# Kernel optimization log

Measured on AMD Instinct MI355X. Metric: run time of the kernel, lower is better.

Reference implementation:

```python
import jax, jax.numpy as jnp
import numpy as np

D_MODEL = 1024
HEADS = 16
D_K = D_MODEL // HEADS
D_FF = 4096
B, S = 8, 1024
EPS = 1e-5
NEG = -1e9


def layer_norm(x, g, b):
    mu = jnp.mean(x, axis=-1, keepdims=True)
    var = jnp.var(x, axis=-1, keepdims=True)
    return (x - mu) * jax.lax.rsqrt(var + EPS) * g + b


def setup_inputs() -> dict:
    key = jax.random.key(0)
    ks = jax.random.split(key, 10)
    sc = lambda d: 1.0 / np.sqrt(d)
    return {
        "x": jax.random.normal(ks[0], (B, S, D_MODEL), jnp.float32),
        "mask": jnp.ones((B, 1, 1, S), jnp.int32),
        "wq": jax.random.normal(ks[1], (D_MODEL, D_MODEL), jnp.float32) * sc(D_MODEL),
        "bq": jnp.zeros((D_MODEL,), jnp.float32),
        "wk": jax.random.normal(ks[2], (D_MODEL, D_MODEL), jnp.float32) * sc(D_MODEL),
        "bk": jnp.zeros((D_MODEL,), jnp.float32),
        "wv": jax.random.normal(ks[3], (D_MODEL, D_MODEL), jnp.float32) * sc(D_MODEL),
        "bv": jnp.zeros((D_MODEL,), jnp.float32),
        "wo": jax.random.normal(ks[4], (D_MODEL, D_MODEL), jnp.float32) * sc(D_MODEL),
        "bo": jnp.zeros((D_MODEL,), jnp.float32),
        "w1": jax.random.normal(ks[5], (D_MODEL, D_FF), jnp.float32) * sc(D_MODEL),
        "b1": jnp.zeros((D_FF,), jnp.float32),
        "w2": jax.random.normal(ks[6], (D_FF, D_MODEL), jnp.float32) * sc(D_FF),
        "b2": jnp.zeros((D_MODEL,), jnp.float32),
        "ln1_g": jnp.ones((D_MODEL,), jnp.float32),
        "ln1_b": jnp.zeros((D_MODEL,), jnp.float32),
        "ln2_g": jnp.ones((D_MODEL,), jnp.float32),
        "ln2_b": jnp.zeros((D_MODEL,), jnp.float32),
    }


def reference(x, mask, wq, bq, wk, bk, wv, bv, wo, bo, w1, b1, w2, b2,
              ln1_g, ln1_b, ln2_g, ln2_b):
    b, s, d = x.shape

    # --- self-attention sublayer with residual + LN (pre-norm, dropout=0) ---
    h = layer_norm(x, ln1_g, ln1_b)
    q = (h @ wq + bq).reshape(b, s, HEADS, D_K).transpose(0, 2, 1, 3)  # [b,h,s,dk]
    k = (h @ wk + bk).reshape(b, s, HEADS, D_K).transpose(0, 2, 1, 3)
    v = (h @ wv + bv).reshape(b, s, HEADS, D_K).transpose(0, 2, 1, 3)

    scores = jnp.einsum("bhqd,bhkd->bhqk", q, k) / np.sqrt(D_K)  # [b,h,s,s]
    scores = jnp.where(mask == 0, NEG, scores)
    attn = jax.nn.softmax(scores, axis=-1)
    ctx = jnp.einsum("bhqk,bhkd->bhqd", attn, v)
    ctx = ctx.transpose(0, 2, 1, 3).reshape(b, s, d)
    x = x + (ctx @ wo + bo)

    # --- feed-forward sublayer with residual + LN ---
    h2 = layer_norm(x, ln2_g, ln2_b)
    ff = jax.nn.relu(h2 @ w1 + b1) @ w2 + b2
    return x + ff
```

## Files before the change

kernel.cpp:

```cpp
#include <hip/hip_runtime.h>
#include <hip/hip_bf16.h>

typedef __attribute__((ext_vector_type(8))) __bf16 bf16x8;
typedef __attribute__((ext_vector_type(4))) __bf16 bf16x4;
typedef __attribute__((ext_vector_type(4))) float  f32x4;

__device__ __forceinline__ void gload_lds16(const __bf16* g, __bf16* l) {
    __builtin_amdgcn_global_load_lds(
        (const __attribute__((address_space(1))) void*)g,
        (__attribute__((address_space(3))) void*)l, 16, 0, 0);
}

__global__ __launch_bounds__(256) void transpose_all(
    const float* __restrict__ wq, const float* __restrict__ wk,
    const float* __restrict__ wv, const float* __restrict__ wo,
    const float* __restrict__ w1, const float* __restrict__ w2,
    __bf16* __restrict__ wqkvT, __bf16* __restrict__ woT,
    __bf16* __restrict__ w1T, __bf16* __restrict__ w2T) {
    __shared__ float t[32][33];
    const int bid = blockIdx.x;
    const float* in; __bf16* out; int K, N, nb, kb;
    if (bid < 4096) {
        const int which = bid >> 10, tt = bid & 1023;
        K = 1024; N = 1024;
        in  = which == 0 ? wq : which == 1 ? wk : which == 2 ? wv : wo;
        out = which == 3 ? woT : wqkvT + (size_t)which * 1048576;
        nb = (tt & 31) * 32; kb = (tt >> 5) * 32;
    } else if (bid < 8192) {
        const int tt = bid - 4096;
        in = w1; out = w1T; K = 1024; N = 4096;
        nb = (tt & 127) * 32; kb = (tt >> 7) * 32;
    } else {
        const int tt = bid - 8192;
        in = w2; out = w2T; K = 4096; N = 1024;
        nb = (tt & 31) * 32; kb = (tt >> 5) * 32;
    }
    const int tx = threadIdx.x & 31, ty = threadIdx.x >> 5;
#pragma unroll
    for (int i = 0; i < 32; i += 8)
        t[ty + i][tx] = in[(size_t)(kb + ty + i) * N + nb + tx];
    __syncthreads();
#pragma unroll
    for (int i = 0; i < 32; i += 8)
        out[(size_t)(nb + ty + i) * K + kb + tx] = (__bf16)t[tx][ty + i];
}

__global__ void concat3(const float* __restrict__ a, const float* __restrict__ b,
                        const float* __restrict__ c, float* __restrict__ o, int n) {
    int i = blockIdx.x * 256 + threadIdx.x;
    if (i < n) { o[i] = a[i]; o[n + i] = b[i]; o[2 * n + i] = c[i]; }
}

__global__ __launch_bounds__(256) void ln_to_bf16(const float* __restrict__ x,
                                                  const float* __restrict__ g,
                                                  const float* __restrict__ bb,
                                                  __bf16* __restrict__ out) {
    const int row = blockIdx.x, t = threadIdx.x;
    const float4 v = ((const float4*)(x + (size_t)row * 1024))[t];
    float s  = v.x + v.y + v.z + v.w;
    float ss = v.x * v.x + v.y * v.y + v.z * v.z + v.w * v.w;
#pragma unroll
    for (int off = 32; off; off >>= 1) {
        s  += __shfl_down(s, off);
        ss += __shfl_down(ss, off);
    }
    __shared__ float ps[4], pss[4];
    if ((t & 63) == 0) { ps[t >> 6] = s; pss[t >> 6] = ss; }
    __syncthreads();
    s  = ps[0] + ps[1] + ps[2] + ps[3];
    ss = pss[0] + pss[1] + pss[2] + pss[3];
    const float mu   = s * (1.0f / 1024.0f);
    const float var  = ss * (1.0f / 1024.0f) - mu * mu;
    const float rinv = rsqrtf(var + 1e-5f);
    const float4 gv = ((const float4*)g)[t];
    const float4 bv = ((const float4*)bb)[t];
    bf16x4 o;
    o[0] = (__bf16)((v.x - mu) * rinv * gv.x + bv.x);
    o[1] = (__bf16)((v.y - mu) * rinv * gv.y + bv.y);
    o[2] = (__bf16)((v.z - mu) * rinv * gv.z + bv.z);
    o[3] = (__bf16)((v.w - mu) * rinv * gv.w + bv.w);
    *(bf16x4*)(out + (size_t)row * 1024 + 4 * t) = o;
}

template <int MODE>
__global__ __launch_bounds__(512, 2) void gemm256(const __bf16* __restrict__ A,
                                                  const __bf16* __restrict__ BT,
                                                  const float* __restrict__ bias,
                                                  __bf16* __restrict__ outp,
                                                  int M, int N, int K, int NMB) {
    __shared__ __align__(16) __bf16 lds[65536];
    const int nwg = gridDim.x;
    const int bid = blockIdx.x;
    const int wgid = (bid & 7) * (nwg >> 3) + (bid >> 3);
    const int bm = (wgid % NMB) * 256, bn = (wgid / NMB) * 256;
    const int tid = threadIdx.x, l = tid & 63, w = tid >> 6;
    const int wm = (w >> 2) * 128, wn = (w & 3) * 64;
    const int lg = l >> 4, lm = l & 15;
    const int NT = K >> 6;

    const __bf16* gsrc[4];
    int ldst[4];
#pragma unroll
    for (int j = 0; j < 4; ++j) {
        const unsigned X = (unsigned)(((j & 1) << 13) + (w << 10) + l * 16);
        const unsigned L = X ^ (((X >> 7) & 7u) << 4);
        const int row = L >> 6, col = (L & 63) >> 1;
        gsrc[j] = (j < 2 ? A + (size_t)(bm + row) * K : BT + (size_t)(bn + row) * K) + col;
        ldst[j] = ((j < 2 ? 0 : 16384) + ((j & 1) << 13) + (w << 10)) >> 1;
    }
    int aoff[2][4], boff[4];
#pragma unroll
    for (int mh = 0; mh < 2; ++mh)
#pragma unroll
        for (int fr = 0; fr < 4; ++fr) {
            const unsigned Lb = (unsigned)(wm + mh * 64 + fr * 16 + lm) * 64 + lg * 16;
            aoff[mh][fr] = (int)(Lb ^ (((Lb >> 7) & 7u) << 4)) >> 1;
        }
#pragma unroll
    for (int n = 0; n < 4; ++n) {
        const unsigned Lb = (unsigned)(wn + n * 16 + lm) * 64 + lg * 16;
        boff[n] = (int)(16384u + (Lb ^ (((Lb >> 7) & 7u) << 4))) >> 1;
    }

    f32x4 acc[8][4];
#pragma unroll
    for (int m = 0; m < 8; ++m)
#pragma unroll
        for (int n = 0; n < 4; ++n) acc[m][n] = f32x4{0.f, 0.f, 0.f, 0.f};

#define ISSUE_SUB(u)                                                          \
    do {                                                                      \
        __bf16* sbp = lds + (((u) & 3) << 14);                                \
        const int go = (u) << 5;                                              \
        _Pragma("unroll")                                                     \
        for (int j = 0; j < 4; ++j) gload_lds16(gsrc[j] + go, sbp + ldst[j]); \
    } while (0)

#define MFMA16(MH, BREG)                                                      \
    do {                                                                      \
        __builtin_amdgcn_s_setprio(1);                                        \
        _Pragma("unroll")                                                     \
        for (int i = 0; i < 4; ++i)                                           \
            _Pragma("unroll")                                                 \
            for (int n = 0; n < 4; ++n)                                       \
                acc[(MH)*4 + i][n] = __builtin_amdgcn_mfma_f32_16x16x32_bf16( \
                    af[i], BREG[n], acc[(MH)*4 + i][n], 0, 0, 0);             \
        __builtin_amdgcn_s_setprio(0);                                        \
    } while (0)

    ISSUE_SUB(0); ISSUE_SUB(1); ISSUE_SUB(2); ISSUE_SUB(3);
    asm volatile("s_waitcnt vmcnt(8)" ::: "memory");
    __builtin_amdgcn_s_barrier();

    for (int t = 0; t < NT; ++t) {
        const int sa = ((2 * t) & 3) << 14, sb = ((2 * t + 1) & 3) << 14;
        bf16x8 af[4], b0[4], b1[4];
#pragma unroll
        for (int fr = 0; fr < 4; ++fr) af[fr] = *(const bf16x8*)(lds + sa + aoff[0][fr]);
#pragma unroll
        for (int n = 0; n < 4; ++n) b0[n] = *(const bf16x8*)(lds + sa + boff[n]);
        asm volatile("" ::: "memory");
        __builtin_amdgcn_s_barrier();
        __builtin_amdgcn_sched_barrier(0);
        MFMA16(0, b0);
        __builtin_amdgcn_sched_barrier(0);
        __builtin_amdgcn_s_barrier();
#pragma unroll
        for (int fr = 0; fr < 4; ++fr) af[fr] = *(const bf16x8*)(lds + sa + aoff[1][fr]);
        asm volatile("" ::: "memory");
        __builtin_amdgcn_s_barrier();
        __builtin_amdgcn_sched_barrier(0);
        MFMA16(1, b0);
        __builtin_amdgcn_sched_barrier(0);
        __builtin_amdgcn_s_barrier();
        if (t < NT - 2) ISSUE_SUB(2 * t + 4);
#pragma unroll
        for (int fr = 0; fr < 4; ++fr) af[fr] = *(const bf16x8*)(lds + sb + aoff[0][fr]);
#pragma unroll
        for (int n = 0; n < 4; ++n) b1[n] = *(const bf16x8*)(lds + sb + boff[n]);
        asm volatile("" ::: "memory");
        __builtin_amdgcn_s_barrier();
        __builtin_amdgcn_sched_barrier(0);
        MFMA16(0, b1);
        __builtin_amdgcn_sched_barrier(0);
        __builtin_amdgcn_s_barrier();
#pragma unroll
        for (int fr = 0; fr < 4; ++fr) af[fr] = *(const bf16x8*)(lds + sb + aoff[1][fr]);
        asm volatile("" ::: "memory");
        __builtin_amdgcn_s_barrier();
        __builtin_amdgcn_sched_barrier(0);
        MFMA16(1, b1);
        __builtin_amdgcn_sched_barrier(0);
        __builtin_amdgcn_s_barrier();
        if (t < NT - 2) {
            ISSUE_SUB(2 * t + 5);
            asm volatile("s_waitcnt vmcnt(8)" ::: "memory");
        } else if (t == NT - 2) {
            asm volatile("s_waitcnt vmcnt(0)" ::: "memory");
        }
        __builtin_amdgcn_s_barrier();
    }
#undef ISSUE_SUB
#undef MFMA16

#pragma unroll
    for (int m = 0; m < 8; ++m) {
        const int row = bm + wm + (m >> 2) * 64 + (m & 3) * 16 + lg * 4;
#pragma unroll
        for (int n = 0; n < 4; ++n) {
            const int col = bn + wn + n * 16 + lm;
            const float bvv = bias[col];
#pragma unroll
            for (int r = 0; r < 4; ++r) {
                const float v = acc[m][n][r] + bvv;
                outp[(size_t)(row + r) * N + col] =
                    (MODE == 1) ? (__bf16)fmaxf(v, 0.f) : (__bf16)v;
            }
        }
    }
}

__global__ __launch_bounds__(512, 2) void gemm256x128(const __bf16* __restrict__ A,
                                                      const __bf16* __restrict__ BT,
                                                      const float* __restrict__ bias,
                                                      const float* __restrict__ resid,
                                                      float* __restrict__ outp,
                                                      int M, int N, int K, int NMB) {
    __shared__ __align__(16) __bf16 lds[49152];
    const int nwg = gridDim.x;
    const int bid = blockIdx.x;
    const int wgid = (bid & 7) * (nwg >> 3) + (bid >> 3);
    const int bm = (wgid % NMB) * 256, bn = (wgid / NMB) * 128;
    const int tid = threadIdx.x, l = tid & 63, w = tid >> 6;
    const int wm = (w >> 1) * 64, wn = (w & 1) * 64;
    const int lg = l >> 4, lm = l & 15;
    const int NT = K >> 6;

    const __bf16* gsrc[3];
    int ldst[3];
#pragma unroll
    for (int j = 0; j < 3; ++j) {
        const unsigned X = (unsigned)((j == 1 ? 8192 : 0) + tid * 16);
        const unsigned L = X ^ (((X >> 7) & 7u) << 4);
        const int row = L >> 6, col = (L & 63) >> 1;
        gsrc[j] = (j < 2 ? A + (size_t)(bm + row) * K : BT + (size_t)(bn + row) * K) + col;
        ldst[j] = ((j < 2 ? (j << 13) : 16384) + (w << 10)) >> 1;
    }
    int aoff[2][2], boff[4];
#pragma unroll
    for (int mh = 0; mh < 2; ++mh)
#pragma unroll
        for (int fr = 0; fr < 2; ++fr) {
            const unsigned Lb = (unsigned)(wm + mh * 32 + fr * 16 + lm) * 64 + lg * 16;
            aoff[mh][fr] = (int)(Lb ^ (((Lb >> 7) & 7u) << 4)) >> 1;
        }
#pragma unroll
    for (int n = 0; n < 4; ++n) {
        const unsigned Lb = (unsigned)(wn + n * 16 + lm) * 64 + lg * 16;
        boff[n] = (int)(16384u + (Lb ^ (((Lb >> 7) & 7u) << 4))) >> 1;
    }

    f32x4 acc[4][4];
#pragma unroll
    for (int m = 0; m < 4; ++m)
#pragma unroll
        for (int n = 0; n < 4; ++n) acc[m][n] = f32x4{0.f, 0.f, 0.f, 0.f};

#define ISSUE_SUB(u)                                                          \
    do {                                                                      \
        __bf16* sbp = lds + ((u) & 3) * 12288;                                \
        const int go = (u) << 5;                                              \
        _Pragma("unroll")                                                     \
        for (int j = 0; j < 3; ++j) gload_lds16(gsrc[j] + go, sbp + ldst[j]); \
    } while (0)

#define MFMA8(MH, BREG)                                                       \
    do {                                                                      \
        __builtin_amdgcn_s_setprio(1);                                        \
        _Pragma("unroll")                                                     \
        for (int i = 0; i < 2; ++i)                                           \
            _Pragma("unroll")                                                 \
            for (int n = 0; n < 4; ++n)                                       \
                acc[(MH)*2 + i][n] = __builtin_amdgcn_mfma_f32_16x16x32_bf16( \
                    af[i], BREG[n], acc[(MH)*2 + i][n], 0, 0, 0);             \
        __builtin_amdgcn_s_setprio(0);                                        \
    } while (0)

    ISSUE_SUB(0); ISSUE_SUB(1); ISSUE_SUB(2); ISSUE_SUB(3);
    asm volatile("s_waitcnt vmcnt(6)" ::: "memory");
    __builtin_amdgcn_s_barrier();

    for (int t = 0; t < NT; ++t) {
        const int sa = ((2 * t) & 3) * 12288, sb = ((2 * t + 1) & 3) * 12288;
        bf16x8 af[2], b0[4], b1[4];
#pragma unroll
        for (int fr = 0; fr < 2; ++fr) af[fr] = *(const bf16x8*)(lds + sa + aoff[0][fr]);
#pragma unroll
        for (int n = 0; n < 4; ++n) b0[n] = *(const bf16x8*)(lds + sa + boff[n]);
        asm volatile("" ::: "memory");
        __builtin_amdgcn_s_barrier();
        __builtin_amdgcn_sched_barrier(0);
        MFMA8(0, b0);
        __builtin_amdgcn_sched_barrier(0);
        __builtin_amdgcn_s_barrier();
#pragma unroll
        for (int fr = 0; fr < 2; ++fr) af[fr] = *(const bf16x8*)(lds + sa + aoff[1][fr]);
        asm volatile("" ::: "memory");
        __builtin_amdgcn_s_barrier();
        __builtin_amdgcn_sched_barrier(0);
        MFMA8(1, b0);
        __builtin_amdgcn_sched_barrier(0);
        __builtin_amdgcn_s_barrier();
        if (t < NT - 2) ISSUE_SUB(2 * t + 4);
#pragma unroll
        for (int fr = 0; fr < 2; ++fr) af[fr] = *(const bf16x8*)(lds + sb + aoff[0][fr]);
#pragma unroll
        for (int n = 0; n < 4; ++n) b1[n] = *(const bf16x8*)(lds + sb + boff[n]);
        asm volatile("" ::: "memory");
        __builtin_amdgcn_s_barrier();
        __builtin_amdgcn_sched_barrier(0);
        MFMA8(0, b1);
        __builtin_amdgcn_sched_barrier(0);
        __builtin_amdgcn_s_barrier();
#pragma unroll
        for (int fr = 0; fr < 2; ++fr) af[fr] = *(const bf16x8*)(lds + sb + aoff[1][fr]);
        asm volatile("" ::: "memory");
        __builtin_amdgcn_s_barrier();
        __builtin_amdgcn_sched_barrier(0);
        MFMA8(1, b1);
        __builtin_amdgcn_sched_barrier(0);
        __builtin_amdgcn_s_barrier();
        if (t < NT - 2) {
            ISSUE_SUB(2 * t + 5);
            asm volatile("s_waitcnt vmcnt(6)" ::: "memory");
        } else if (t == NT - 2) {
            asm volatile("s_waitcnt vmcnt(0)" ::: "memory");
        }
        __builtin_amdgcn_s_barrier();
    }
#undef ISSUE_SUB
#undef MFMA8

#pragma unroll
    for (int m = 0; m < 4; ++m) {
        const int row = bm + wm + m * 16 + lg * 4;
#pragma unroll
        for (int n = 0; n < 4; ++n) {
            const int col = bn + wn + n * 16 + lm;
            const float bvv = bias[col];
#pragma unroll
            for (int r = 0; r < 4; ++r) {
                const size_t idx = (size_t)(row + r) * N + col;
                outp[idx] = resid[idx] + acc[m][n][r] + bvv;
            }
        }
    }
}

__global__ __launch_bounds__(512, 2) void gemm_qkv(const __bf16* __restrict__ A,
                                                   const __bf16* __restrict__ BT,
                                                   const float* __restrict__ bias,
                                                   __bf16* __restrict__ outp,
                                                   __bf16* __restrict__ vTout,
                                                   int M, int N, int K, int NMB) {
    __shared__ __align__(16) __bf16 lds[49152];
    const int nwg = gridDim.x;
    const int bid = blockIdx.x;
    const int wgid = (bid & 7) * (nwg >> 3) + (bid >> 3);
    const int bm = (wgid % NMB) * 128, bn = (wgid / NMB) * 256;
    const int tid = threadIdx.x, l = tid & 63, w = tid >> 6;
    const int wm = (w >> 2) * 64, wn = (w & 3) * 64;
    const int lg = l >> 4, lm = l & 15;
    const int NT = K >> 6;

    const __bf16* gsrc[3];
    int ldst[3];
#pragma unroll
    for (int j = 0; j < 3; ++j) {
        const unsigned X = (unsigned)((j == 0 ? 0 : (j - 1) * 8192) + tid * 16);
        const unsigned L = X ^ (((X >> 7) & 7u) << 4);
        const int row = L >> 6, col = (L & 63) >> 1;
        gsrc[j] = (j == 0 ? A + (size_t)(bm + row) * K : BT + (size_t)(bn + row) * K) + col;
        ldst[j] = ((j == 0 ? 0 : 8192 + (j - 1) * 8192) + (w << 10)) >> 1;
    }
    int aoff[2][2], boff[4];
#pragma unroll
    for (int mh = 0; mh < 2; ++mh)
#pragma unroll
        for (int fr = 0; fr < 2; ++fr) {
            const unsigned Lb = (unsigned)(wm + mh * 32 + fr * 16 + lm) * 64 + lg * 16;
            aoff[mh][fr] = (int)(Lb ^ (((Lb >> 7) & 7u) << 4)) >> 1;
        }
#pragma unroll
    for (int n = 0; n < 4; ++n) {
        const unsigned Lb = (unsigned)(wn + n * 16 + lm) * 64 + lg * 16;
        boff[n] = (int)(8192u + (Lb ^ (((Lb >> 7) & 7u) << 4))) >> 1;
    }

    f32x4 acc[4][4];
#pragma unroll
    for (int m = 0; m < 4; ++m)
#pragma unroll
        for (int n = 0; n < 4; ++n) acc[m][n] = f32x4{0.f, 0.f, 0.f, 0.f};

#define ISSUE_SUB(u)                                                          \
    do {                                                                      \
        __bf16* sbp = lds + ((u) & 3) * 12288;                                \
        const int go = (u) << 5;                                              \
        _Pragma("unroll")                                                     \
        for (int j = 0; j < 3; ++j) gload_lds16(gsrc[j] + go, sbp + ldst[j]); \
    } while (0)

#define MFMA8(MH, BREG)                                                       \
    do {                                                                      \
        __builtin_amdgcn_s_setprio(1);                                        \
        _Pragma("unroll")                                                     \
        for (int i = 0; i < 2; ++i)                                           \
            _Pragma("unroll")                                                 \
            for (int n = 0; n < 4; ++n)                                       \
                acc[(MH)*2 + i][n] = __builtin_amdgcn_mfma_f32_16x16x32_bf16( \
                    af[i], BREG[n], acc[(MH)*2 + i][n], 0, 0, 0);             \
        __builtin_amdgcn_s_setprio(0);                                        \
    } while (0)

    ISSUE_SUB(0); ISSUE_SUB(1); ISSUE_SUB(2); ISSUE_SUB(3);
    asm volatile("s_waitcnt vmcnt(6)" ::: "memory");
    __builtin_amdgcn_s_barrier();

    for (int t = 0; t < NT; ++t) {
        const int sa = ((2 * t) & 3) * 12288, sb = ((2 * t + 1) & 3) * 12288;
        bf16x8 af[2], b0[4], b1[4];
#pragma unroll
        for (int fr = 0; fr < 2; ++fr) af[fr] = *(const bf16x8*)(lds + sa + aoff[0][fr]);
#pragma unroll
        for (int n = 0; n < 4; ++n) b0[n] = *(const bf16x8*)(lds + sa + boff[n]);
        asm volatile("" ::: "memory");
        __builtin_amdgcn_s_barrier();
        __builtin_amdgcn_sched_barrier(0);
        MFMA8(0, b0);
        __builtin_amdgcn_sched_barrier(0);
        __builtin_amdgcn_s_barrier();
#pragma unroll
        for (int fr = 0; fr < 2; ++fr) af[fr] = *(const bf16x8*)(lds + sa + aoff[1][fr]);
        asm volatile("" ::: "memory");
        __builtin_amdgcn_s_barrier();
        __builtin_amdgcn_sched_barrier(0);
        MFMA8(1, b0);
        __builtin_amdgcn_sched_barrier(0);
        __builtin_amdgcn_s_barrier();
        if (t < NT - 2) ISSUE_SUB(2 * t + 4);
#pragma unroll
        for (int fr = 0; fr < 2; ++fr) af[fr] = *(const bf16x8*)(lds + sb + aoff[0][fr]);
#pragma unroll
        for (int n = 0; n < 4; ++n) b1[n] = *(const bf16x8*)(lds + sb + boff[n]);
        asm volatile("" ::: "memory");
        __builtin_amdgcn_s_barrier();
        __builtin_amdgcn_sched_barrier(0);
        MFMA8(0, b1);
        __builtin_amdgcn_sched_barrier(0);
        __builtin_amdgcn_s_barrier();
#pragma unroll
        for (int fr = 0; fr < 2; ++fr) af[fr] = *(const bf16x8*)(lds + sb + aoff[1][fr]);
        asm volatile("" ::: "memory");
        __builtin_amdgcn_s_barrier();
        __builtin_amdgcn_sched_barrier(0);
        MFMA8(1, b1);
        __builtin_amdgcn_sched_barrier(0);
        __builtin_amdgcn_s_barrier();
        if (t < NT - 2) {
            ISSUE_SUB(2 * t + 5);
            asm volatile("s_waitcnt vmcnt(6)" ::: "memory");
        } else if (t == NT - 2) {
            asm volatile("s_waitcnt vmcnt(0)" ::: "memory");
        }
        __builtin_amdgcn_s_barrier();
    }
#undef ISSUE_SUB
#undef MFMA8

    const bool isQ = bn < 1024;
#pragma unroll
    for (int m = 0; m < 4; ++m) {
        const int row = bm + wm + m * 16 + lg * 4;
#pragma unroll
        for (int n = 0; n < 4; ++n) {
            const int col = bn + wn + n * 16 + lm;
            const float bvv = bias[col];
            if (bn >= 2048) {
                bf16x4 o;
#pragma unroll
                for (int r = 0; r < 4; ++r) o[r] = (__bf16)(acc[m][n][r] + bvv);
                *(bf16x4*)(vTout + (size_t)((row >> 10) * 1024 + (col - 2048)) * 1024 +
                           (row & 1023)) = o;
            } else {
#pragma unroll
                for (int r = 0; r < 4; ++r) {
                    float v = acc[m][n][r] + bvv;
                    if (isQ) v *= 0.18033688f;
                    outp[(size_t)(row + r) * 2048 + col] = (__bf16)v;
                }
            }
        }
    }
}

__global__ __launch_bounds__(512) void attn_kernel(const __bf16* __restrict__ qk,
                                                   const __bf16* __restrict__ vT,
                                                   const int* __restrict__ mask,
                                                   __bf16* __restrict__ ctx) {
    const int qt = blockIdx.x, h = blockIdx.y, b = blockIdx.z;
    const int tid = threadIdx.x, w = tid >> 6, l = tid & 63;
    const int lg = l >> 4, lm = l & 15;

    __shared__ __align__(16) __bf16 Ks[2][64][76];
    __shared__ __align__(16) __bf16 Vt[2][64][76];
    __shared__ __align__(16) __bf16 Ps[8][16][76];

    const int qrow = qt * 128 + w * 16 + lm;
    const __bf16* qp = qk + (size_t)(b * 1024 + qrow) * 2048 + h * 64 + lg * 8;
    bf16x8 aq[2];
    aq[0] = *(const bf16x8*)qp;
    aq[1] = *(const bf16x8*)(qp + 32);

    const int r0 = tid >> 3, cc0 = (tid & 7) * 8;
    const __bf16* kbase = qk + (size_t)(b * 1024 + r0) * 2048 + 1024 + h * 64 + cc0;
    const __bf16* vbase = vT + (size_t)(b * 1024 + h * 64 + r0) * 1024 + cc0;
    uint4 kreg, vreg;
#define ALOAD(kt)                                                      \
    do {                                                               \
        kreg = *(const uint4*)(kbase + (size_t)(kt) * 64 * 2048);      \
        vreg = *(const uint4*)(vbase + (kt) * 64);                     \
    } while (0)
#define AWRITE(bf)                                                     \
    do {                                                               \
        *(uint4*)&Ks[bf][r0][cc0] = kreg;                              \
        *(uint4*)&Vt[bf][r0][cc0] = vreg;                              \
    } while (0)

    ALOAD(0); AWRITE(0); ALOAD(1);
    __syncthreads();

    const int* mbase = mask + b * 1024;
    float mrun = -1e30f, lsum = 0.f;
    f32x4 oacc[4];
#pragma unroll
    for (int n = 0; n < 4; ++n) oacc[n] = f32x4{0.f, 0.f, 0.f, 0.f};

    for (int kt = 0; kt < 16; ++kt) {
        const int cur = kt & 1;
        f32x4 sacc[4];
        int4 mk4[4];
#pragma unroll
        for (int n = 0; n < 4; ++n) {
            mk4[n] = *(const int4*)(mbase + kt * 64 + n * 16 + lg * 4);
            sacc[n] = f32x4{0.f, 0.f, 0.f, 0.f};
#pragma unroll
            for (int kk = 0; kk < 2; ++kk) {
                bf16x8 bk = *(const bf16x8*)&Ks[cur][n * 16 + lm][lg * 8 + kk * 32];
                sacc[n] = __builtin_amdgcn_mfma_f32_16x16x32_bf16(bk, aq[kk], sacc[n], 0, 0, 0);
            }
        }
        float p[4][4], mn[4];
#pragma unroll
        for (int n = 0; n < 4; ++n) {
            p[n][0] = mk4[n].x ? sacc[n][0] : -1e9f;
            p[n][1] = mk4[n].y ? sacc[n][1] : -1e9f;
            p[n][2] = mk4[n].z ? sacc[n][2] : -1e9f;
            p[n][3] = mk4[n].w ? sacc[n][3] : -1e9f;
            mn[n] = fmaxf(fmaxf(p[n][0], p[n][1]), fmaxf(p[n][2], p[n][3]));
        }
        float mloc = fmaxf(fmaxf(mn[0], mn[1]), fmaxf(mn[2], mn[3]));
        mloc = fmaxf(mloc, __shfl_xor(mloc, 16));
        mloc = fmaxf(mloc, __shfl_xor(mloc, 32));
        const float pm = fmaxf(mrun, mloc);
        if (!__all(pm - mrun <= 11.5f)) {
            const float sc = exp2f(mrun - pm);
            mrun = pm;
            lsum *= sc;
            float scr[4];
#pragma unroll
            for (int r = 0; r < 4; ++r) scr[r] = __shfl(sc, lg * 4 + r);
#pragma unroll
            for (int n = 0; n < 4; ++n)
#pragma unroll
                for (int r = 0; r < 4; ++r) oacc[n][r] *= scr[r];
        }
        float rsn[4];
#pragma unroll
        for (int n = 0; n < 4; ++n) {
#pragma unroll
            for (int r = 0; r < 4; ++r) p[n][r] = exp2f(p[n][r] - mrun);
            rsn[n] = (p[n][0] + p[n][1]) + (p[n][2] + p[n][3]);
        }
        float rs = (rsn[0] + rsn[1]) + (rsn[2] + rsn[3]);
        rs += __shfl_xor(rs, 16);
        rs += __shfl_xor(rs, 32);
        lsum += rs;
#pragma unroll
        for (int n = 0; n < 4; ++n) {
            bf16x4 pb;
#pragma unroll
            for (int r = 0; r < 4; ++r) pb[r] = (__bf16)p[n][r];
            *(bf16x4*)&Ps[w][lm][n * 16 + lg * 4] = pb;
        }
        bf16x8 ap[2];
        ap[0] = *(const bf16x8*)&Ps[w][lm][lg * 8];
        ap[1] = *(const bf16x8*)&Ps[w][lm][lg * 8 + 32];
#pragma unroll
        for (int n = 0; n < 4; ++n)
#pragma unroll
            for (int kk = 0; kk < 2; ++kk) {
                bf16x8 bv = *(const bf16x8*)&Vt[cur][n * 16 + lm][lg * 8 + kk * 32];
                oacc[n] = __builtin_amdgcn_mfma_f32_16x16x32_bf16(ap[kk], bv, oacc[n], 0, 0, 0);
            }
        __syncthreads();
        if (kt < 15) AWRITE(cur ^ 1);
        if (kt < 14) ALOAD(kt + 2);
        __syncthreads();
    }
#undef ALOAD
#undef AWRITE
    float lsr[4];
#pragma unroll
    for (int r = 0; r < 4; ++r) lsr[r] = __shfl(lsum, lg * 4 + r);
#pragma unroll
    for (int n = 0; n < 4; ++n)
#pragma unroll
        for (int r = 0; r < 4; ++r) {
            const float val = oacc[n][r] / lsr[r];
            const int row = qt * 128 + w * 16 + lg * 4 + r;
            ctx[(size_t)(b * 1024 + row) * 1024 + h * 64 + n * 16 + lm] = (__bf16)val;
        }
}

extern "C" void kernel_launch(void* const* d_in, const int* in_sizes, int n_in,
                              void* d_out, int out_size, void* d_ws, size_t ws_size,
                              hipStream_t stream) {
    const float* x    = (const float*)d_in[0];
    const int*   mask = (const int*)d_in[1];
    const float* wq   = (const float*)d_in[2];
    const float* bq   = (const float*)d_in[3];
    const float* wk   = (const float*)d_in[4];
    const float* bk   = (const float*)d_in[5];
    const float* wv   = (const float*)d_in[6];
    const float* bv   = (const float*)d_in[7];
    const float* wo   = (const float*)d_in[8];
    const float* bo   = (const float*)d_in[9];
    const float* w1   = (const float*)d_in[10];
    const float* b1   = (const float*)d_in[11];
    const float* w2   = (const float*)d_in[12];
    const float* b2   = (const float*)d_in[13];
    const float* ln1g = (const float*)d_in[14];
    const float* ln1b = (const float*)d_in[15];
    const float* ln2g = (const float*)d_in[16];
    const float* ln2b = (const float*)d_in[17];
    float* out = (float*)d_out;
    char* ws = (char*)d_ws;

    __bf16* wqkvT = (__bf16*)(ws + 0);
    __bf16* woT   = (__bf16*)(ws + 6291456);
    __bf16* w1T   = (__bf16*)(ws + 8388608);
    __bf16* w2T   = (__bf16*)(ws + 16777216);
    float*  bqkv  = (float*)(ws + 25165824);
    __bf16* hb    = (__bf16*)(ws + 25178112);
    __bf16* qkb   = (__bf16*)(ws + 41955328);
    __bf16* vTb   = (__bf16*)(ws + 75509760);
    __bf16* ctxb  = (__bf16*)(ws + 92286976);
    __bf16* ff1b  = qkb;

    transpose_all<<<12288, 256, 0, stream>>>(wq, wk, wv, wo, w1, w2,
                                             wqkvT, woT, w1T, w2T);
    concat3<<<4, 256, 0, stream>>>(bq, bk, bv, bqkv, 1024);

    ln_to_bf16<<<8192, 256, 0, stream>>>(x, ln1g, ln1b, hb);
    gemm_qkv<<<768, 512, 0, stream>>>(hb, wqkvT, bqkv, qkb, vTb, 8192, 3072, 1024, 64);
    attn_kernel<<<dim3(8, 16, 8), 512, 0, stream>>>(qkb, vTb, mask, ctxb);
    gemm256x128<<<256, 512, 0, stream>>>(ctxb, woT, bo, x, out, 8192, 1024, 1024, 32);
    ln_to_bf16<<<8192, 256, 0, stream>>>(out, ln2g, ln2b, hb);
    gemm256<1><<<512, 512, 0, stream>>>(hb, w1T, b1, ff1b, 8192, 4096, 1024, 32);
    gemm256x128<<<256, 512, 0, stream>>>(ff1b, w2T, b2, out, out, 8192, 1024, 4096, 32);
}
```

Measured before the change: 394.6 us.

## Keep attention P in registers via shuffles, remap GEMM tiles per XCD, reorder attention grid

The attention kernel drops the per-wave LDS staging of the probability tile. It builds the MFMA operand with cross-lane shuffles and computes the transposed product (V^T·P) so each lane owns one query row. This removes the per-row rescale shuffles and allows vectorized context stores. The next K/V tile prefetch now starts at the top of each iteration, one barrier is removed, and the launch bound requests 6 waves per SIMD. All GEMMs get a new tile mapping that gives each of the 8 XCDs a contiguous band of M rows, for better L2 reuse. The attention grid is reordered so heads vary fastest.

Result: faster. 379.2 us (-3.9%).

```diff
diff --git a/kernel.cpp b/kernel.cpp
--- a/kernel.cpp
+++ b/kernel.cpp
@@ -89,10 +89,11 @@
                                                   __bf16* __restrict__ outp,
                                                   int M, int N, int K, int NMB) {
     __shared__ __align__(16) __bf16 lds[65536];
-    const int nwg = gridDim.x;
     const int bid = blockIdx.x;
-    const int wgid = (bid & 7) * (nwg >> 3) + (bid >> 3);
-    const int bm = (wgid % NMB) * 256, bn = (wgid / NMB) * 256;
+    const int c8 = bid & 7, loc = bid >> 3;
+    const int MH = NMB >> 3;
+    const int bm = (c8 * MH + loc % MH) * 256;
+    const int bn = (loc / MH) * 256;
     const int tid = threadIdx.x, l = tid & 63, w = tid >> 6;
     const int wm = (w >> 2) * 128, wn = (w & 3) * 64;
     const int lg = l >> 4, lm = l & 15;
@@ -136,15 +137,15 @@
         for (int j = 0; j < 4; ++j) gload_lds16(gsrc[j] + go, sbp + ldst[j]); \
     } while (0)
 
-#define MFMA16(MH, BREG)                                                      \
+#define MFMA16(MH_, BREG)                                                     \
     do {                                                                      \
         __builtin_amdgcn_s_setprio(1);                                        \
         _Pragma("unroll")                                                     \
         for (int i = 0; i < 4; ++i)                                           \
             _Pragma("unroll")                                                 \
             for (int n = 0; n < 4; ++n)                                       \
-                acc[(MH)*4 + i][n] = __builtin_amdgcn_mfma_f32_16x16x32_bf16( \
-                    af[i], BREG[n], acc[(MH)*4 + i][n], 0, 0, 0);             \
+                acc[(MH_)*4 + i][n] = __builtin_amdgcn_mfma_f32_16x16x32_bf16(\
+                    af[i], BREG[n], acc[(MH_)*4 + i][n], 0, 0, 0);            \
         __builtin_amdgcn_s_setprio(0);                                        \
     } while (0)
 
@@ -227,10 +228,11 @@
                                                       float* __restrict__ outp,
                                                       int M, int N, int K, int NMB) {
     __shared__ __align__(16) __bf16 lds[49152];
-    const int nwg = gridDim.x;
     const int bid = blockIdx.x;
-    const int wgid = (bid & 7) * (nwg >> 3) + (bid >> 3);
-    const int bm = (wgid % NMB) * 256, bn = (wgid / NMB) * 128;
+    const int c8 = bid & 7, loc = bid >> 3;
+    const int MH = NMB >> 3;
+    const int bm = (c8 * MH + loc % MH) * 256;
+    const int bn = (loc / MH) * 128;
     const int tid = threadIdx.x, l = tid & 63, w = tid >> 6;
     const int wm = (w >> 1) * 64, wn = (w & 1) * 64;
     const int lg = l >> 4, lm = l & 15;
@@ -274,15 +276,15 @@
         for (int j = 0; j < 3; ++j) gload_lds16(gsrc[j] + go, sbp + ldst[j]); \
     } while (0)
 
-#define MFMA8(MH, BREG)                                                       \
+#define MFMA8(MH_, BREG)                                                      \
     do {                                                                      \
         __builtin_amdgcn_s_setprio(1);                                        \
         _Pragma("unroll")                                                     \
         for (int i = 0; i < 2; ++i)                                           \
             _Pragma("unroll")                                                 \
             for (int n = 0; n < 4; ++n)                                       \
-                acc[(MH)*2 + i][n] = __builtin_amdgcn_mfma_f32_16x16x32_bf16( \
-                    af[i], BREG[n], acc[(MH)*2 + i][n], 0, 0, 0);             \
+                acc[(MH_)*2 + i][n] = __builtin_amdgcn_mfma_f32_16x16x32_bf16(\
+                    af[i], BREG[n], acc[(MH_)*2 + i][n], 0, 0, 0);            \
         __builtin_amdgcn_s_setprio(0);                                        \
     } while (0)
 
@@ -364,10 +366,11 @@
                                                    __bf16* __restrict__ vTout,
                                                    int M, int N, int K, int NMB) {
     __shared__ __align__(16) __bf16 lds[49152];
-    const int nwg = gridDim.x;
     const int bid = blockIdx.x;
-    const int wgid = (bid & 7) * (nwg >> 3) + (bid >> 3);
-    const int bm = (wgid % NMB) * 128, bn = (wgid / NMB) * 256;
+    const int c8 = bid & 7, loc = bid >> 3;
+    const int MH = NMB >> 3;
+    const int bm = (c8 * MH + loc % MH) * 128;
+    const int bn = (loc / MH) * 256;
     const int tid = threadIdx.x, l = tid & 63, w = tid >> 6;
     const int wm = (w >> 2) * 64, wn = (w & 3) * 64;
     const int lg = l >> 4, lm = l & 15;
@@ -411,15 +414,15 @@
         for (int j = 0; j < 3; ++j) gload_lds16(gsrc[j] + go, sbp + ldst[j]); \
     } while (0)
 
-#define MFMA8(MH, BREG)                                                       \
+#define MFMA8(MH_, BREG)                                                      \
     do {                                                                      \
         __builtin_amdgcn_s_setprio(1);                                        \
         _Pragma("unroll")                                                     \
         for (int i = 0; i < 2; ++i)                                           \
             _Pragma("unroll")                                                 \
             for (int n = 0; n < 4; ++n)                                       \
-                acc[(MH)*2 + i][n] = __builtin_amdgcn_mfma_f32_16x16x32_bf16( \
-                    af[i], BREG[n], acc[(MH)*2 + i][n], 0, 0, 0);             \
+                acc[(MH_)*2 + i][n] = __builtin_amdgcn_mfma_f32_16x16x32_bf16(\
+                    af[i], BREG[n], acc[(MH_)*2 + i][n], 0, 0, 0);            \
         __builtin_amdgcn_s_setprio(0);                                        \
     } while (0)
 
@@ -504,17 +507,16 @@
     }
 }
 
-__global__ __launch_bounds__(512) void attn_kernel(const __bf16* __restrict__ qk,
-                                                   const __bf16* __restrict__ vT,
-                                                   const int* __restrict__ mask,
-                                                   __bf16* __restrict__ ctx) {
-    const int qt = blockIdx.x, h = blockIdx.y, b = blockIdx.z;
+__global__ __launch_bounds__(512, 6) void attn_kernel(const __bf16* __restrict__ qk,
+                                                      const __bf16* __restrict__ vT,
+                                                      const int* __restrict__ mask,
+                                                      __bf16* __restrict__ ctx) {
+    const int h = blockIdx.x, qt = blockIdx.y, b = blockIdx.z;
     const int tid = threadIdx.x, w = tid >> 6, l = tid & 63;
     const int lg = l >> 4, lm = l & 15;
 
     __shared__ __align__(16) __bf16 Ks[2][64][76];
     __shared__ __align__(16) __bf16 Vt[2][64][76];
-    __shared__ __align__(16) __bf16 Ps[8][16][76];
 
     const int qrow = qt * 128 + w * 16 + lm;
     const __bf16* qp = qk + (size_t)(b * 1024 + qrow) * 2048 + h * 64 + lg * 8;
@@ -541,6 +543,7 @@
     __syncthreads();
 
     const int* mbase = mask + b * 1024;
+    const int srcA = ((lg & 1) << 5) + lm, srcB = srcA + 16;
     float mrun = -1e30f, lsum = 0.f;
     f32x4 oacc[4];
 #pragma unroll
@@ -548,6 +551,8 @@
 
     for (int kt = 0; kt < 16; ++kt) {
         const int cur = kt & 1;
+        if (kt < 15) AWRITE(cur ^ 1);
+        if (kt < 14) ALOAD(kt + 2);
         f32x4 sacc[4];
         int4 mk4[4];
 #pragma unroll
@@ -577,13 +582,10 @@
             const float sc = exp2f(mrun - pm);
             mrun = pm;
             lsum *= sc;
-            float scr[4];
-#pragma unroll
-            for (int r = 0; r < 4; ++r) scr[r] = __shfl(sc, lg * 4 + r);
 #pragma unroll
             for (int n = 0; n < 4; ++n)
 #pragma unroll
-                for (int r = 0; r < 4; ++r) oacc[n][r] *= scr[r];
+                for (int r = 0; r < 4; ++r) oacc[n][r] *= sc;
         }
         float rsn[4];
 #pragma unroll
@@ -597,40 +599,44 @@
         rs += __shfl_xor(rs, 32);
         lsum += rs;
 #pragma unroll
-        for (int n = 0; n < 4; ++n) {
-            bf16x4 pb;
-#pragma unroll
-            for (int r = 0; r < 4; ++r) pb[r] = (__bf16)p[n][r];
-            *(bf16x4*)&Ps[w][lm][n * 16 + lg * 4] = pb;
-        }
-        bf16x8 ap[2];
-        ap[0] = *(const bf16x8*)&Ps[w][lm][lg * 8];
-        ap[1] = *(const bf16x8*)&Ps[w][lm][lg * 8 + 32];
-#pragma unroll
-        for (int n = 0; n < 4; ++n)
-#pragma unroll
-            for (int kk = 0; kk < 2; ++kk) {
-                bf16x8 bv = *(const bf16x8*)&Vt[cur][n * 16 + lm][lg * 8 + kk * 32];
-                oacc[n] = __builtin_amdgcn_mfma_f32_16x16x32_bf16(ap[kk], bv, oacc[n], 0, 0, 0);
+        for (int kk = 0; kk < 2; ++kk) {
+            bf16x4 pb0, pb1;
+#pragma unroll
+            for (int r = 0; r < 4; ++r) {
+                pb0[r] = (__bf16)p[2 * kk][r];
+                pb1[r] = (__bf16)p[2 * kk + 1][r];
             }
-        __syncthreads();
-        if (kt < 15) AWRITE(cur ^ 1);
-        if (kt < 14) ALOAD(kt + 2);
+            const uint2 u0 = *(const uint2*)&pb0;
+            const uint2 u1 = *(const uint2*)&pb1;
+            const int a0 = __shfl((int)u0.x, srcA), a1 = __shfl((int)u0.y, srcA);
+            const int a2 = __shfl((int)u0.x, srcB), a3 = __shfl((int)u0.y, srcB);
+            const int c0 = __shfl((int)u1.x, srcA), c1 = __shfl((int)u1.y, srcA);
+            const int c2 = __shfl((int)u1.x, srcB), c3 = __shfl((int)u1.y, srcB);
+            uint4 pf;
+            const bool hi = (lg & 2) != 0;
+            pf.x = hi ? c0 : a0;
+            pf.y = hi ? c1 : a1;
+            pf.z = hi ? c2 : a2;
+            pf.w = hi ? c3 : a3;
+            const bf16x8 pfrag = *(const bf16x8*)&pf;
+#pragma unroll
+            for (int nd = 0; nd < 4; ++nd) {
+                bf16x8 vf = *(const bf16x8*)&Vt[cur][nd * 16 + lm][lg * 8 + kk * 32];
+                oacc[nd] = __builtin_amdgcn_mfma_f32_16x16x32_bf16(vf, pfrag, oacc[nd], 0, 0, 0);
+            }
+        }
         __syncthreads();
     }
 #undef ALOAD
 #undef AWRITE
-    float lsr[4];
-#pragma unroll
-    for (int r = 0; r < 4; ++r) lsr[r] = __shfl(lsum, lg * 4 + r);
-#pragma unroll
-    for (int n = 0; n < 4; ++n)
-#pragma unroll
-        for (int r = 0; r < 4; ++r) {
-            const float val = oacc[n][r] / lsr[r];
-            const int row = qt * 128 + w * 16 + lg * 4 + r;
-            ctx[(size_t)(b * 1024 + row) * 1024 + h * 64 + n * 16 + lm] = (__bf16)val;
-        }
+    const float rinv = 1.0f / lsum;
+#pragma unroll
+    for (int nd = 0; nd < 4; ++nd) {
+        bf16x4 o;
+#pragma unroll
+        for (int r = 0; r < 4; ++r) o[r] = (__bf16)(oacc[nd][r] * rinv);
+        *(bf16x4*)(ctx + (size_t)(b * 1024 + qrow) * 1024 + h * 64 + nd * 16 + lg * 4) = o;
+    }
 }
 
 extern "C" void kernel_launch(void* const* d_in, const int* in_sizes, int n_in,
@@ -674,7 +680,7 @@
 
     ln_to_bf16<<<8192, 256, 0, stream>>>(x, ln1g, ln1b, hb);
     gemm_qkv<<<768, 512, 0, stream>>>(hb, wqkvT, bqkv, qkb, vTb, 8192, 3072, 1024, 64);
-    attn_kernel<<<dim3(8, 16, 8), 512, 0, stream>>>(qkb, vTb, mask, ctxb);
+    attn_kernel<<<dim3(16, 8, 8), 512, 0, stream>>>(qkb, vTb, mask, ctxb);
     gemm256x128<<<256, 512, 0, stream>>>(ctxb, woT, bo, x, out, 8192, 1024, 1024, 32);
     ln_to_bf16<<<8192, 256, 0, stream>>>(out, ln2g, ln2b, hb);
     gemm256<1><<<512, 512, 0, stream>>>(hb, w1T, b1, ff1b, 8192, 4096, 1024, 32);
```
